# Optimization experiments

Measured on AMD Instinct MI355X. Metric: run time of the kernel, lower is better.

The kernel has to match this reference:

```python
import jax, jax.numpy as jnp
import numpy as np
from jax import lax

S, B, V, E, H = 512, 64, 50000, 400, 1150


def _lstm_layer(x, h0, c0, Wih, Whh, bih, bhh):
    # x: [S, B, Din]; PyTorch LSTM gate order: i, f, g, o
    WihT, WhhT = Wih.T, Whh.T

    def step(carry, xt):
        h, c = carry
        gates = xt @ WihT + bih + h @ WhhT + bhh  # [B, 4*Dh]
        i, f, g, o = jnp.split(gates, 4, axis=-1)
        c_new = jax.nn.sigmoid(f) * c + jax.nn.sigmoid(i) * jnp.tanh(g)
        h_new = jax.nn.sigmoid(o) * jnp.tanh(c_new)
        return (h_new, c_new), h_new

    (_, _), ys = lax.scan(step, (h0, c0), x)
    return ys  # [S, B, Dh]


def setup_inputs() -> dict:
    key = jax.random.key(0)

    def u(i, shape, s):
        return jax.random.uniform(jax.random.fold_in(key, i), shape, jnp.float32, -s, s)

    inp = {"tokens": jax.random.randint(jax.random.fold_in(key, 0), (S, B), 0, V)}
    inp["emb_w"] = u(1, (V, E), 0.1)  # encoder.weight.uniform_(-0.1, 0.1)
    dims = [(E, H), (H, H), (H, E)]  # (input_size, hidden_size) per layer
    k = 2
    for l, (din, dh) in enumerate(dims):
        s = 1.0 / float(np.sqrt(dh))
        inp[f"Wih{l}"] = u(k, (4 * dh, din), s); k += 1
        inp[f"Whh{l}"] = u(k, (4 * dh, dh), s); k += 1
        inp[f"bih{l}"] = u(k, (4 * dh,), s); k += 1
        inp[f"bhh{l}"] = u(k, (4 * dh,), s); k += 1
        inp[f"h{l}"] = jnp.zeros((B, dh), jnp.float32)
        inp[f"c{l}"] = jnp.zeros((B, dh), jnp.float32)
    return inp


def reference(tokens, emb_w, Wih0, Whh0, bih0, bhh0, Wih1, Whh1, bih1, bhh1,
              Wih2, Whh2, bih2, bhh2, h0, c0, h1, c1, h2, c2):
    # Eval-mode forward: embedding/locked/weight dropouts are identity.
    x = emb_w[tokens]  # [S, B, E]
    x = _lstm_layer(x, h0, c0, Wih0, Whh0, bih0, bhh0)  # [S, B, H]
    x = _lstm_layer(x, h1, c1, Wih1, Whh1, bih1, bhh1)  # [S, B, H]
    x = _lstm_layer(x, h2, c2, Wih2, Whh2, bih2, bhh2)  # [S, B, E]
    return x
```

## Files before the change

### kernel.cpp

```cpp
#include <hip/hip_runtime.h>
#include <hip/hip_bf16.h>
#include <cstdint>
#include <cstddef>


typedef _Float16 f16x8 __attribute__((ext_vector_type(8)));
typedef float f32x4 __attribute__((ext_vector_type(4)));
typedef unsigned int u32x4 __attribute__((ext_vector_type(4)));

#define LSTM_NBLK   241
#define LSTM_WSTEPS 515
#define LDS_W_HALFS (4 * 36 * 64 * 8)
#define LDS_TOTAL_BYTES (LDS_W_HALFS * 2 + 16384)
#define GO_BASE 248

struct KParams {
  const unsigned short* res[3];
  const unsigned short* strm[3];
  const float* bias[3];
  const unsigned short* xin0;
  unsigned short* ring[3];
  float* part;
  float* out;
  int* bar;
};

__device__ __forceinline__ float sigm_(float x) { return 1.0f / (1.0f + __expf(-x)); }
__device__ __forceinline__ float tanh_(float x) { return 2.0f * sigm_(2.0f * x) - 1.0f; }
__device__ __forceinline__ unsigned short f2h(float x) {
  _Float16 h = (_Float16)x;
  return __builtin_bit_cast(unsigned short, h);
}
__device__ __forceinline__ u32x4 load_sc(const unsigned short* p) {
  u32x4 r;
  asm volatile("global_load_dwordx4 %0, %1, off sc0 sc1"
               : "=v"(r) : "v"(p) : "memory");
  return r;
}
__device__ __forceinline__ f32x4 load_sc128f(const float* p) {
  f32x4 r;
  asm volatile("global_load_dwordx4 %0, %1, off sc0 sc1"
               : "=v"(r) : "v"(p) : "memory");
  return r;
}
__device__ __forceinline__ void store_sc128(unsigned short* p, u32x4 v) {
  asm volatile("global_store_dwordx4 %0, %1, off sc0 sc1" :: "v"(p), "v"(v) : "memory");
}
__device__ __forceinline__ void store_sc128f(float* p, f32x4 v) {
  asm volatile("global_store_dwordx4 %0, %1, off sc0 sc1" :: "v"(p), "v"(v) : "memory");
}
__device__ __forceinline__ void store_sc_i(int* p, int v) {
  asm volatile("global_store_dword %0, %1, off sc0 sc1" :: "v"(p), "v"(v) : "memory");
}
__device__ __forceinline__ int load_sc_i(const int* p) {
  int v;
  asm volatile("global_load_dword %0, %1, off sc0 sc1\n\ts_waitcnt vmcnt(0)"
               : "=v"(v) : "v"(p) : "memory");
  __builtin_amdgcn_sched_barrier(0);
  return v;
}
__device__ __forceinline__ void wait_vm0() {
  asm volatile("s_waitcnt vmcnt(0)" ::: "memory");
  __builtin_amdgcn_sched_barrier(0);
}

__device__ __forceinline__ void grid_barrier(int* bar, int bid, int tid, int tau1) {
  wait_vm0();
  __syncthreads();
  if (bid == 0) {
    if (tid >= 1 && tid < LSTM_NBLK) {
      int guard = 0;
      while (load_sc_i(&bar[tid * 32]) < tau1 && ++guard < (1 << 20))
        __builtin_amdgcn_s_sleep(1);
    }
    __syncthreads();
    if (tid < 8) store_sc_i(&bar[(GO_BASE + tid) * 32], tau1);
  } else {
    if (tid == 0) {
      store_sc_i(&bar[bid * 32], tau1);
      int guard = 0;
      while (load_sc_i(&bar[(GO_BASE + (bid & 7)) * 32]) < tau1 && ++guard < (1 << 20))
        __builtin_amdgcn_s_sleep(1);
    }
    __syncthreads();
  }
}

template<int L, int LAG>
__device__ __forceinline__ void run_layer(const KParams& p, int g, int bid,
                                          unsigned short* ldsW, float* gates) {
  constexpr int DH    = (L == 2) ? 400 : 1150;
  constexpr int NKB1  = (L == 0) ? 13 : 36;
  constexpr int NKB2  = (L == 2) ? 13 : 36;
  constexpr int XSTR  = (L == 0) ? 416 : 1152;
  constexpr int HSTR  = (L == 2) ? 416 : 1152;
  constexpr bool B1_RES = (L == 2);
  constexpr int NKB_ST = B1_RES ? NKB2 : NKB1;

  const unsigned short* __restrict__ strm = p.strm[L] + (size_t)g * (4 * NKB_ST * 512);
  const float* __restrict__ bias          = p.bias[L];
  const unsigned short* __restrict__ xin  = (L == 0) ? p.xin0 : p.ring[L - 1];
  unsigned short* __restrict__ own        = p.ring[L];

  const int tid  = threadIdx.x;
  const int lane = tid & 63;
  const int w    = tid >> 6;
  const int m0   = (w >> 2) << 4;
  const int kq   = w & 3;
  const int r    = lane & 15;
  const int q    = lane >> 4;

  {
    const uint4* src = (const uint4*)(p.res[L] + (size_t)g * LDS_W_HALFS);
    uint4* dst = (uint4*)ldsW;
    for (int i = tid; i < LDS_W_HALFS / 8; i += 1024) dst[i] = src[i];
#pragma unroll
    for (int s2 = 0; s2 < 4; ++s2) gates[s2 * 1024 + tid] = 0.0f;
  }

  const int b_ = tid >> 4;
  const int jp = tid & 15;
  const int jglob = g * 16 + jp;
  float bias4[4];
#pragma unroll
  for (int ss = 0; ss < 4; ++ss) bias4[ss] = bias[ss * 1152 + jglob];
  float c_val = 0.0f;
  __syncthreads();

  for (int tau = 0; tau < LSTM_WSTEPS; ++tau) {
    const int t = tau - LAG;
    if (t >= 0 && t < 512) {
      f32x4 acc[4] = {{0,0,0,0},{0,0,0,0},{0,0,0,0},{0,0,0,0}};

      const size_t slot1 = (L == 0) ? (size_t)t : (size_t)((t + 1) & 7);
      const unsigned short* a1base = xin + slot1 * (64 * XSTR) + (size_t)(m0 + r) * XSTR + q * 8;
      const unsigned short* a2base = own + (size_t)(t & 7) * (64 * HSTR) + (size_t)(m0 + r) * HSTR + q * 8;

      u32x4 a1r[9]; u32x4 a2r[9];
      if constexpr (L != 0) {
#pragma unroll
        for (int i = 0; i < 9; ++i) {
          int kb = kq + 4 * i;
          if (NKB1 == 36 || kb < NKB1) a1r[i] = load_sc(a1base + kb * 32);
        }
      }
#pragma unroll
      for (int i = 0; i < 9; ++i) {
        int kb = kq + 4 * i;
        if (i < ((NKB2 == 36) ? 9 : 4) && (NKB2 == 36 || kb < NKB2))
          a2r[i] = load_sc(a2base + kb * 32);
      }
      wait_vm0();

#pragma unroll
      for (int i = 0; i < ((NKB1 == 36) ? 9 : 4); ++i) {
        int kb = kq + 4 * i;
        if (NKB1 == 36 || kb < NKB1) {
          f16x8 a = (L == 0) ? *(const f16x8*)(a1base + kb * 32)
                             : __builtin_bit_cast(f16x8, a1r[i]);
#pragma unroll
          for (int s2 = 0; s2 < 4; ++s2) {
            f16x8 b = B1_RES
              ? *(const f16x8*)&ldsW[((s2 * 36 + kb) * 64 + lane) * 8]
              : *(const f16x8*)&strm[((size_t)(s2 * NKB_ST + kb) * 64 + lane) * 8];
            acc[s2] = __builtin_amdgcn_mfma_f32_16x16x32_f16(a, b, acc[s2], 0, 0, 0);
          }
        }
      }
#pragma unroll
      for (int i = 0; i < ((NKB2 == 36) ? 9 : 4); ++i) {
        int kb = kq + 4 * i;
        if (NKB2 == 36 || kb < NKB2) {
          f16x8 a = __builtin_bit_cast(f16x8, a2r[i]);
#pragma unroll
          for (int s2 = 0; s2 < 4; ++s2) {
            f16x8 b = B1_RES
              ? *(const f16x8*)&strm[((size_t)(s2 * NKB_ST + kb) * 64 + lane) * 8]
              : *(const f16x8*)&ldsW[((s2 * 36 + kb) * 64 + lane) * 8];
            acc[s2] = __builtin_amdgcn_mfma_f32_16x16x32_f16(a, b, acc[s2], 0, 0, 0);
          }
        }
      }

#pragma unroll
      for (int s2 = 0; s2 < 4; ++s2)
#pragma unroll
        for (int i = 0; i < 4; ++i)
          atomicAdd(&gates[s2 * 1024 + (m0 + q * 4 + i) * 16 + r], acc[s2][i]);
      __syncthreads();

      float pg[4];
#pragma unroll
      for (int s2 = 0; s2 < 4; ++s2) {
        pg[s2] = gates[s2 * 1024 + tid];
        gates[s2 * 1024 + tid] = 0.0f;
      }
      float ig = sigm_(pg[0] + bias4[0]);
      float fg = sigm_(pg[1] + bias4[1]);
      float gg = tanh_(pg[2] + bias4[2]);
      float og = sigm_(pg[3] + bias4[3]);
      c_val = fg * c_val + ig * gg;
      float h = og * tanh_(c_val);
      if (jglob >= DH) h = 0.0f;

      unsigned v0  = (unsigned)f2h(h);
      unsigned o1  = __shfl_down(v0, 1);
      unsigned p01 = v0 | (o1 << 16);
      unsigned o2  = __shfl_down(p01, 2);
      unsigned o4a = __shfl_down(p01, 4);
      unsigned o4b = __shfl_down(o2, 4);
      if ((lane & 7) == 0) {
        u32x4 pk; pk[0] = p01; pk[1] = o2; pk[2] = o4a; pk[3] = o4b;
        store_sc128(own + (size_t)(((t + 1) & 7) * 64 + b_) * HSTR + jglob, pk);
      }
      if (L == 2 && jglob < DH)
        p.out[((size_t)t * 64 + b_) * 400 + jglob] = h;
    }
    grid_barrier(p.bar, bid, tid, tau + 1);
  }
}

__device__ __forceinline__ void run_l1_ih(const KParams& p, int g, int bid,
                                          unsigned short* ldsW, float* gates) {
  const unsigned short* __restrict__ xin = p.ring[0];
  const int tid  = threadIdx.x;
  const int lane = tid & 63;
  const int w    = tid >> 6;
  const int m0   = (w >> 2) << 4;
  const int kq   = w & 3;
  const int r    = lane & 15;
  const int q    = lane >> 4;

  {
    const uint4* src = (const uint4*)(p.strm[1] + (size_t)g * LDS_W_HALFS);
    uint4* dst = (uint4*)ldsW;
    for (int i = tid; i < LDS_W_HALFS / 8; i += 1024) dst[i] = src[i];
#pragma unroll
    for (int s2 = 0; s2 < 4; ++s2) gates[s2 * 1024 + tid] = 0.0f;
  }
  __syncthreads();

  for (int tau = 0; tau < LSTM_WSTEPS; ++tau) {
    const int t = tau - 1;
    if (t >= 0 && t < 512) {
      f32x4 acc[4] = {{0,0,0,0},{0,0,0,0},{0,0,0,0},{0,0,0,0}};
      const unsigned short* a1base =
          xin + (size_t)((t + 1) & 7) * (64 * 1152) + (size_t)(m0 + r) * 1152 + q * 8;
      u32x4 a1r[9];
#pragma unroll
      for (int i = 0; i < 9; ++i) a1r[i] = load_sc(a1base + (kq + 4 * i) * 32);
      wait_vm0();
#pragma unroll
      for (int i = 0; i < 9; ++i) {
        int kb = kq + 4 * i;
        f16x8 a = __builtin_bit_cast(f16x8, a1r[i]);
#pragma unroll
        for (int s2 = 0; s2 < 4; ++s2) {
          f16x8 b = *(const f16x8*)&ldsW[((s2 * 36 + kb) * 64 + lane) * 8];
          acc[s2] = __builtin_amdgcn_mfma_f32_16x16x32_f16(a, b, acc[s2], 0, 0, 0);
        }
      }
#pragma unroll
      for (int s2 = 0; s2 < 4; ++s2)
#pragma unroll
        for (int i = 0; i < 4; ++i)
          atomicAdd(&gates[s2 * 1024 + (m0 + q * 4 + i) * 16 + r], acc[s2][i]);
      __syncthreads();
      f32x4 pk;
#pragma unroll
      for (int s2 = 0; s2 < 4; ++s2) {
        pk[s2] = gates[s2 * 1024 + tid];
        gates[s2 * 1024 + tid] = 0.0f;
      }
      store_sc128f(p.part + ((size_t)((t & 1) * 72 + g) * 1024 + tid) * 4, pk);
    }
    grid_barrier(p.bar, bid, tid, tau + 1);
  }
}

__device__ __forceinline__ void run_l1_hh(const KParams& p, int g, int bid,
                                          unsigned short* ldsW, float* gates) {
  unsigned short* __restrict__ own = p.ring[1];
  const int tid  = threadIdx.x;
  const int lane = tid & 63;
  const int w    = tid >> 6;
  const int m0   = (w >> 2) << 4;
  const int kq   = w & 3;
  const int r    = lane & 15;
  const int q    = lane >> 4;

  {
    const uint4* src = (const uint4*)(p.res[1] + (size_t)g * LDS_W_HALFS);
    uint4* dst = (uint4*)ldsW;
    for (int i = tid; i < LDS_W_HALFS / 8; i += 1024) dst[i] = src[i];
#pragma unroll
    for (int s2 = 0; s2 < 4; ++s2) gates[s2 * 1024 + tid] = 0.0f;
  }

  const int b_ = tid >> 4;
  const int jp = tid & 15;
  const int jglob = g * 16 + jp;
  float bias4[4];
#pragma unroll
  for (int ss = 0; ss < 4; ++ss) bias4[ss] = p.bias[1][ss * 1152 + jglob];
  float c_val = 0.0f;
  __syncthreads();

  for (int tau = 0; tau < LSTM_WSTEPS; ++tau) {
    const int t = tau - 2;
    if (t >= 0 && t < 512) {
      f32x4 acc[4] = {{0,0,0,0},{0,0,0,0},{0,0,0,0},{0,0,0,0}};
      const unsigned short* a2base =
          own + (size_t)(t & 7) * (64 * 1152) + (size_t)(m0 + r) * 1152 + q * 8;
      u32x4 a2r[9];
#pragma unroll
      for (int i = 0; i < 9; ++i) a2r[i] = load_sc(a2base + (kq + 4 * i) * 32);
      f32x4 pl = load_sc128f(p.part + ((size_t)((t & 1) * 72 + g) * 1024 + tid) * 4);
      wait_vm0();
#pragma unroll
      for (int i = 0; i < 9; ++i) {
        int kb = kq + 4 * i;
        f16x8 a = __builtin_bit_cast(f16x8, a2r[i]);
#pragma unroll
        for (int s2 = 0; s2 < 4; ++s2) {
          f16x8 b = *(const f16x8*)&ldsW[((s2 * 36 + kb) * 64 + lane) * 8];
          acc[s2] = __builtin_amdgcn_mfma_f32_16x16x32_f16(a, b, acc[s2], 0, 0, 0);
        }
      }
#pragma unroll
      for (int s2 = 0; s2 < 4; ++s2)
#pragma unroll
        for (int i = 0; i < 4; ++i)
          atomicAdd(&gates[s2 * 1024 + (m0 + q * 4 + i) * 16 + r], acc[s2][i]);
      __syncthreads();

      float pg[4];
#pragma unroll
      for (int s2 = 0; s2 < 4; ++s2) {
        pg[s2] = gates[s2 * 1024 + tid];
        gates[s2 * 1024 + tid] = 0.0f;
      }
      float ig = sigm_(pg[0] + pl[0] + bias4[0]);
      float fg = sigm_(pg[1] + pl[1] + bias4[1]);
      float gg = tanh_(pg[2] + pl[2] + bias4[2]);
      float og = sigm_(pg[3] + pl[3] + bias4[3]);
      c_val = fg * c_val + ig * gg;
      float h = og * tanh_(c_val);
      if (jglob >= 1150) h = 0.0f;

      unsigned v0  = (unsigned)f2h(h);
      unsigned o1  = __shfl_down(v0, 1);
      unsigned p01 = v0 | (o1 << 16);
      unsigned o2  = __shfl_down(p01, 2);
      unsigned o4a = __shfl_down(p01, 4);
      unsigned o4b = __shfl_down(o2, 4);
      if ((lane & 7) == 0) {
        u32x4 pk2; pk2[0] = p01; pk2[1] = o2; pk2[2] = o4a; pk2[3] = o4b;
        store_sc128(own + (size_t)(((t + 1) & 7) * 64 + b_) * 1152 + jglob, pk2);
      }
    }
    grid_barrier(p.bar, bid, tid, tau + 1);
  }
}

__global__ void __launch_bounds__(1024) lstm_persistent(KParams p) {
  extern __shared__ unsigned short smem[];
  unsigned short* ldsW = smem;
  float* gates = (float*)(smem + LDS_W_HALFS);
  const int bid = blockIdx.x;
  if (bid < 72)       run_layer<0, 0>(p, bid, bid, ldsW, gates);
  else if (bid < 144) run_l1_ih(p, bid - 72, bid, ldsW, gates);
  else if (bid < 216) run_l1_hh(p, bid - 144, bid, ldsW, gates);
  else                run_layer<2, 3>(p, bid - 216, bid, ldsW, gates);
}

__global__ void prep_weights(const float* __restrict__ src,
                             unsigned short* __restrict__ dst,
                             int Jext, int jg, int K, int NKB) {
  const int n = jg * 4 * NKB * 512;
  for (int idx = blockIdx.x * blockDim.x + threadIdx.x; idx < n;
       idx += gridDim.x * blockDim.x) {
    int e = idx & 7;
    int t2 = idx >> 3;
    int ln = t2 & 63; t2 >>= 6;
    int kb = t2 % NKB; t2 /= NKB;
    int s = t2 & 3;
    int g = t2 >> 2;
    int j = g * 16 + (ln & 15);
    int k = kb * 32 + (ln >> 4) * 8 + e;
    unsigned short v = 0;
    if (j < Jext && k < K) v = f2h(src[(size_t)(s * Jext + j) * K + k]);
    dst[idx] = v;
  }
}

__global__ void prep_bias(const float* __restrict__ bih,
                          const float* __restrict__ bhh,
                          float* __restrict__ dst, int Dh) {
  const int n = 4 * 1152;
  for (int idx = blockIdx.x * blockDim.x + threadIdx.x; idx < n;
       idx += gridDim.x * blockDim.x) {
    int s = idx / 1152, j = idx % 1152;
    float v = 0.0f;
    if (j < Dh) v = bih[s * Dh + j] + bhh[s * Dh + j];
    dst[idx] = v;
  }
}

__global__ void prep_gather(const int* __restrict__ tokens,
                            const float* __restrict__ emb,
                            unsigned short* __restrict__ xin0) {
  const int n = 512 * 64 * 52;
  for (int idx = blockIdx.x * blockDim.x + threadIdx.x; idx < n;
       idx += gridDim.x * blockDim.x) {
    int row = idx / 52;
    int cp  = idx - row * 52;
    unsigned short v[8] = {0, 0, 0, 0, 0, 0, 0, 0};
    if (cp < 50) {
      const float* src = emb + (size_t)tokens[row] * 400 + cp * 8;
      float4 a = *(const float4*)(src);
      float4 b = *(const float4*)(src + 4);
      v[0] = f2h(a.x); v[1] = f2h(a.y); v[2] = f2h(a.z); v[3] = f2h(a.w);
      v[4] = f2h(b.x); v[5] = f2h(b.y); v[6] = f2h(b.z); v[7] = f2h(b.w);
    }
    *(uint4*)(xin0 + (size_t)row * 416 + cp * 8) = *(const uint4*)v;
  }
}

extern "C" void kernel_launch(void* const* d_in, const int* in_sizes, int n_in,
                              void* d_out, int out_size, void* d_ws, size_t ws_size,
                              hipStream_t stream) {
  const int*   tokens = (const int*)d_in[0];
  const float* emb  = (const float*)d_in[1];
  const float* Wih0 = (const float*)d_in[2];
  const float* Whh0 = (const float*)d_in[3];
  const float* bih0 = (const float*)d_in[4];
  const float* bhh0 = (const float*)d_in[5];
  const float* Wih1 = (const float*)d_in[8];
  const float* Whh1 = (const float*)d_in[9];
  const float* bih1 = (const float*)d_in[10];
  const float* bhh1 = (const float*)d_in[11];
  const float* Wih2 = (const float*)d_in[14];
  const float* Whh2 = (const float*)d_in[15];
  const float* bih2 = (const float*)d_in[16];
  const float* bhh2 = (const float*)d_in[17];

  char* ws = (char*)d_ws;
  size_t off = 0;
  auto alloc = [&](size_t bytes) -> char* {
    char* ptr = ws + off;
    off += (bytes + 255) & ~(size_t)255;
    return ptr;
  };
  unsigned short* res0  = (unsigned short*)alloc(72ull * 4 * 36 * 512 * 2);
  unsigned short* res1  = (unsigned short*)alloc(72ull * 4 * 36 * 512 * 2);
  unsigned short* res2  = (unsigned short*)alloc(25ull * 4 * 36 * 512 * 2);
  unsigned short* strm0 = (unsigned short*)alloc(72ull * 4 * 13 * 512 * 2);
  unsigned short* strm1 = (unsigned short*)alloc(72ull * 4 * 36 * 512 * 2);
  unsigned short* strm2 = (unsigned short*)alloc(25ull * 4 * 13 * 512 * 2);
  float* bias0 = (float*)alloc(4ull * 1152 * 4);
  float* bias1 = (float*)alloc(4ull * 1152 * 4);
  float* bias2 = (float*)alloc(4ull * 1152 * 4);
  unsigned short* xin0  = (unsigned short*)alloc(512ull * 64 * 416 * 2);
  unsigned short* ring0 = (unsigned short*)alloc(8ull * 64 * 1152 * 2);
  unsigned short* ring1 = (unsigned short*)alloc(8ull * 64 * 1152 * 2);
  unsigned short* ring2 = (unsigned short*)alloc(8ull * 64 * 416 * 2);
  float* part = (float*)alloc(2ull * 72 * 1024 * 4 * 4);
  int* bar = (int*)alloc((GO_BASE + 8) * 32 * 4);
  if (off > ws_size) return;

  hipLaunchKernelGGL(prep_gather, dim3(2048), dim3(256), 0, stream, tokens, emb, xin0);
  hipLaunchKernelGGL(prep_weights, dim3(4096), dim3(256), 0, stream, Whh0, res0, 1150, 72, 1150, 36);
  hipLaunchKernelGGL(prep_weights, dim3(4096), dim3(256), 0, stream, Whh1, res1, 1150, 72, 1150, 36);
  hipLaunchKernelGGL(prep_weights, dim3(4096), dim3(256), 0, stream, Wih2, res2, 400, 25, 1150, 36);
  hipLaunchKernelGGL(prep_weights, dim3(4096), dim3(256), 0, stream, Wih0, strm0, 1150, 72, 400, 13);
  hipLaunchKernelGGL(prep_weights, dim3(4096), dim3(256), 0, stream, Wih1, strm1, 1150, 72, 1150, 36);
  hipLaunchKernelGGL(prep_weights, dim3(4096), dim3(256), 0, stream, Whh2, strm2, 400, 25, 400, 13);
  hipLaunchKernelGGL(prep_bias, dim3(8), dim3(256), 0, stream, bih0, bhh0, bias0, 1150);
  hipLaunchKernelGGL(prep_bias, dim3(8), dim3(256), 0, stream, bih1, bhh1, bias1, 1150);
  hipLaunchKernelGGL(prep_bias, dim3(8), dim3(256), 0, stream, bih2, bhh2, bias2, 400);
  (void)hipMemsetAsync(ring0, 0, 8ull * 64 * 1152 * 2, stream);
  (void)hipMemsetAsync(ring1, 0, 8ull * 64 * 1152 * 2, stream);
  (void)hipMemsetAsync(ring2, 0, 8ull * 64 * 416 * 2, stream);
  (void)hipMemsetAsync(bar, 0, (GO_BASE + 8) * 32 * 4, stream);

  KParams kp;
  kp.res[0] = res0;  kp.res[1] = res1;  kp.res[2] = res2;
  kp.strm[0] = strm0; kp.strm[1] = strm1; kp.strm[2] = strm2;
  kp.bias[0] = bias0; kp.bias[1] = bias1; kp.bias[2] = bias2;
  kp.xin0 = xin0;
  kp.ring[0] = ring0; kp.ring[1] = ring1; kp.ring[2] = ring2;
  kp.part = part;
  kp.out = (float*)d_out;
  kp.bar = bar;

  (void)hipFuncSetAttribute((const void*)lstm_persistent,
                            hipFuncAttributeMaxDynamicSharedMemorySize,
                            LDS_TOTAL_BYTES);
  hipLaunchKernelGGL(lstm_persistent, dim3(LSTM_NBLK), dim3(1024),
                     LDS_TOTAL_BYTES, stream, kp);
}
```

Measured before the change: 16.36 ms.

## Merge layer-1 input projection into layer-0 blocks to shrink persistent grid

Removes the 72 dedicated layer-1 input-projection blocks. Layer-0 blocks now also compute the previous step's h0 times Wih1 product, reusing the h0 fragments they already load, with the Wih1 weights streamed from global memory. This cuts the grid from 241 to 169 blocks, so fewer participants join each grid barrier. In exchange, each layer-0 block does more MFMA work, has extra syncthreads and streams more weights per step, which may lengthen the critical path of the layer-0 recurrence.

```diff
diff --git a/kernel.cpp b/kernel.cpp
--- a/kernel.cpp
+++ b/kernel.cpp
@@ -8,11 +8,11 @@
 typedef float f32x4 __attribute__((ext_vector_type(4)));
 typedef unsigned int u32x4 __attribute__((ext_vector_type(4)));
 
-#define LSTM_NBLK   241
+#define LSTM_NBLK   169
 #define LSTM_WSTEPS 515
 #define LDS_W_HALFS (4 * 36 * 64 * 8)
 #define LDS_TOTAL_BYTES (LDS_W_HALFS * 2 + 16384)
-#define GO_BASE 248
+#define GO_BASE 176
 
 struct KParams {
   const unsigned short* res[3];
@@ -86,21 +86,13 @@
   }
 }
 
-template<int L, int LAG>
-__device__ __forceinline__ void run_layer(const KParams& p, int g, int bid,
-                                          unsigned short* ldsW, float* gates) {
-  constexpr int DH    = (L == 2) ? 400 : 1150;
-  constexpr int NKB1  = (L == 0) ? 13 : 36;
-  constexpr int NKB2  = (L == 2) ? 13 : 36;
-  constexpr int XSTR  = (L == 0) ? 416 : 1152;
-  constexpr int HSTR  = (L == 2) ? 416 : 1152;
-  constexpr bool B1_RES = (L == 2);
-  constexpr int NKB_ST = B1_RES ? NKB2 : NKB1;
-
-  const unsigned short* __restrict__ strm = p.strm[L] + (size_t)g * (4 * NKB_ST * 512);
-  const float* __restrict__ bias          = p.bias[L];
-  const unsigned short* __restrict__ xin  = (L == 0) ? p.xin0 : p.ring[L - 1];
-  unsigned short* __restrict__ own        = p.ring[L];
+__device__ __forceinline__ void run_l0_merged(const KParams& p, int g, int bid,
+                                              unsigned short* ldsW, float* gates) {
+  const unsigned short* __restrict__ strmA = p.strm[0] + (size_t)g * (4 * 13 * 512);
+  const unsigned short* __restrict__ strmB = p.strm[1] + (size_t)g * (4 * 36 * 512);
+  const float* __restrict__ bias           = p.bias[0];
+  const unsigned short* __restrict__ xin   = p.xin0;
+  unsigned short* __restrict__ own         = p.ring[0];
 
   const int tid  = threadIdx.x;
   const int lane = tid & 63;
@@ -111,7 +103,7 @@
   const int q    = lane >> 4;
 
   {
-    const uint4* src = (const uint4*)(p.res[L] + (size_t)g * LDS_W_HALFS);
+    const uint4* src = (const uint4*)(p.res[0] + (size_t)g * LDS_W_HALFS);
     uint4* dst = (uint4*)ldsW;
     for (int i = tid; i < LDS_W_HALFS / 8; i += 1024) dst[i] = src[i];
 #pragma unroll
@@ -128,151 +120,110 @@
   __syncthreads();
 
   for (int tau = 0; tau < LSTM_WSTEPS; ++tau) {
-    const int t = tau - LAG;
-    if (t >= 0 && t < 512) {
-      f32x4 acc[4] = {{0,0,0,0},{0,0,0,0},{0,0,0,0},{0,0,0,0}};
-
-      const size_t slot1 = (L == 0) ? (size_t)t : (size_t)((t + 1) & 7);
-      const unsigned short* a1base = xin + slot1 * (64 * XSTR) + (size_t)(m0 + r) * XSTR + q * 8;
-      const unsigned short* a2base = own + (size_t)(t & 7) * (64 * HSTR) + (size_t)(m0 + r) * HSTR + q * 8;
-
-      u32x4 a1r[9]; u32x4 a2r[9];
-      if constexpr (L != 0) {
+    const bool doL0 = (tau < 512);
+    const bool doP  = (tau >= 1 && tau <= 512);
+    if (doL0 || doP) {
+      const unsigned short* a2base =
+          own + (size_t)(tau & 7) * (64 * 1152) + (size_t)(m0 + r) * 1152 + q * 8;
+      u32x4 a2r[9];
+#pragma unroll
+      for (int i = 0; i < 9; ++i) a2r[i] = load_sc(a2base + (kq + 4 * i) * 32);
+      wait_vm0();
+
+      f32x4 acc[4]  = {{0,0,0,0},{0,0,0,0},{0,0,0,0},{0,0,0,0}};
+      f32x4 pacc[4] = {{0,0,0,0},{0,0,0,0},{0,0,0,0},{0,0,0,0}};
+
+      if (doL0) {
+        const unsigned short* a1base =
+            xin + (size_t)tau * (64 * 416) + (size_t)(m0 + r) * 416 + q * 8;
+#pragma unroll
+        for (int i = 0; i < 4; ++i) {
+          int kb = kq + 4 * i;
+          if (kb < 13) {
+            f16x8 a = *(const f16x8*)(a1base + kb * 32);
+#pragma unroll
+            for (int s2 = 0; s2 < 4; ++s2) {
+              f16x8 b = *(const f16x8*)&strmA[((size_t)(s2 * 13 + kb) * 64 + lane) * 8];
+              acc[s2] = __builtin_amdgcn_mfma_f32_16x16x32_f16(a, b, acc[s2], 0, 0, 0);
+            }
+          }
+        }
 #pragma unroll
         for (int i = 0; i < 9; ++i) {
           int kb = kq + 4 * i;
-          if (NKB1 == 36 || kb < NKB1) a1r[i] = load_sc(a1base + kb * 32);
-        }
-      }
-#pragma unroll
-      for (int i = 0; i < 9; ++i) {
-        int kb = kq + 4 * i;
-        if (i < ((NKB2 == 36) ? 9 : 4) && (NKB2 == 36 || kb < NKB2))
-          a2r[i] = load_sc(a2base + kb * 32);
-      }
-      wait_vm0();
-
-#pragma unroll
-      for (int i = 0; i < ((NKB1 == 36) ? 9 : 4); ++i) {
-        int kb = kq + 4 * i;
-        if (NKB1 == 36 || kb < NKB1) {
-          f16x8 a = (L == 0) ? *(const f16x8*)(a1base + kb * 32)
-                             : __builtin_bit_cast(f16x8, a1r[i]);
+          f16x8 a = __builtin_bit_cast(f16x8, a2r[i]);
 #pragma unroll
           for (int s2 = 0; s2 < 4; ++s2) {
-            f16x8 b = B1_RES
-              ? *(const f16x8*)&ldsW[((s2 * 36 + kb) * 64 + lane) * 8]
-              : *(const f16x8*)&strm[((size_t)(s2 * NKB_ST + kb) * 64 + lane) * 8];
+            f16x8 b = *(const f16x8*)&ldsW[((s2 * 36 + kb) * 64 + lane) * 8];
             acc[s2] = __builtin_amdgcn_mfma_f32_16x16x32_f16(a, b, acc[s2], 0, 0, 0);
           }
         }
       }
-#pragma unroll
-      for (int i = 0; i < ((NKB2 == 36) ? 9 : 4); ++i) {
-        int kb = kq + 4 * i;
-        if (NKB2 == 36 || kb < NKB2) {
+      if (doP) {
+#pragma unroll
+        for (int i = 0; i < 9; ++i) {
+          int kb = kq + 4 * i;
           f16x8 a = __builtin_bit_cast(f16x8, a2r[i]);
 #pragma unroll
           for (int s2 = 0; s2 < 4; ++s2) {
-            f16x8 b = B1_RES
-              ? *(const f16x8*)&strm[((size_t)(s2 * NKB_ST + kb) * 64 + lane) * 8]
-              : *(const f16x8*)&ldsW[((s2 * 36 + kb) * 64 + lane) * 8];
-            acc[s2] = __builtin_amdgcn_mfma_f32_16x16x32_f16(a, b, acc[s2], 0, 0, 0);
+            f16x8 b = *(const f16x8*)&strmB[((size_t)(s2 * 36 + kb) * 64 + lane) * 8];
+            pacc[s2] = __builtin_amdgcn_mfma_f32_16x16x32_f16(a, b, pacc[s2], 0, 0, 0);
           }
         }
       }
 
-#pragma unroll
-      for (int s2 = 0; s2 < 4; ++s2)
-#pragma unroll
-        for (int i = 0; i < 4; ++i)
-          atomicAdd(&gates[s2 * 1024 + (m0 + q * 4 + i) * 16 + r], acc[s2][i]);
+      if (doL0) {
+#pragma unroll
+        for (int s2 = 0; s2 < 4; ++s2)
+#pragma unroll
+          for (int i = 0; i < 4; ++i)
+            atomicAdd(&gates[s2 * 1024 + (m0 + q * 4 + i) * 16 + r], acc[s2][i]);
+      }
       __syncthreads();
-
-      float pg[4];
-#pragma unroll
-      for (int s2 = 0; s2 < 4; ++s2) {
-        pg[s2] = gates[s2 * 1024 + tid];
-        gates[s2 * 1024 + tid] = 0.0f;
-      }
-      float ig = sigm_(pg[0] + bias4[0]);
-      float fg = sigm_(pg[1] + bias4[1]);
-      float gg = tanh_(pg[2] + bias4[2]);
-      float og = sigm_(pg[3] + bias4[3]);
-      c_val = fg * c_val + ig * gg;
-      float h = og * tanh_(c_val);
-      if (jglob >= DH) h = 0.0f;
-
-      unsigned v0  = (unsigned)f2h(h);
-      unsigned o1  = __shfl_down(v0, 1);
-      unsigned p01 = v0 | (o1 << 16);
-      unsigned o2  = __shfl_down(p01, 2);
-      unsigned o4a = __shfl_down(p01, 4);
-      unsigned o4b = __shfl_down(o2, 4);
-      if ((lane & 7) == 0) {
-        u32x4 pk; pk[0] = p01; pk[1] = o2; pk[2] = o4a; pk[3] = o4b;
-        store_sc128(own + (size_t)(((t + 1) & 7) * 64 + b_) * HSTR + jglob, pk);
-      }
-      if (L == 2 && jglob < DH)
-        p.out[((size_t)t * 64 + b_) * 400 + jglob] = h;
-    }
-    grid_barrier(p.bar, bid, tid, tau + 1);
-  }
-}
-
-__device__ __forceinline__ void run_l1_ih(const KParams& p, int g, int bid,
-                                          unsigned short* ldsW, float* gates) {
-  const unsigned short* __restrict__ xin = p.ring[0];
-  const int tid  = threadIdx.x;
-  const int lane = tid & 63;
-  const int w    = tid >> 6;
-  const int m0   = (w >> 2) << 4;
-  const int kq   = w & 3;
-  const int r    = lane & 15;
-  const int q    = lane >> 4;
-
-  {
-    const uint4* src = (const uint4*)(p.strm[1] + (size_t)g * LDS_W_HALFS);
-    uint4* dst = (uint4*)ldsW;
-    for (int i = tid; i < LDS_W_HALFS / 8; i += 1024) dst[i] = src[i];
-#pragma unroll
-    for (int s2 = 0; s2 < 4; ++s2) gates[s2 * 1024 + tid] = 0.0f;
-  }
-  __syncthreads();
-
-  for (int tau = 0; tau < LSTM_WSTEPS; ++tau) {
-    const int t = tau - 1;
-    if (t >= 0 && t < 512) {
-      f32x4 acc[4] = {{0,0,0,0},{0,0,0,0},{0,0,0,0},{0,0,0,0}};
-      const unsigned short* a1base =
-          xin + (size_t)((t + 1) & 7) * (64 * 1152) + (size_t)(m0 + r) * 1152 + q * 8;
-      u32x4 a1r[9];
-#pragma unroll
-      for (int i = 0; i < 9; ++i) a1r[i] = load_sc(a1base + (kq + 4 * i) * 32);
-      wait_vm0();
-#pragma unroll
-      for (int i = 0; i < 9; ++i) {
-        int kb = kq + 4 * i;
-        f16x8 a = __builtin_bit_cast(f16x8, a1r[i]);
+      if (doL0) {
+        float pg[4];
 #pragma unroll
         for (int s2 = 0; s2 < 4; ++s2) {
-          f16x8 b = *(const f16x8*)&ldsW[((s2 * 36 + kb) * 64 + lane) * 8];
-          acc[s2] = __builtin_amdgcn_mfma_f32_16x16x32_f16(a, b, acc[s2], 0, 0, 0);
-        }
-      }
-#pragma unroll
-      for (int s2 = 0; s2 < 4; ++s2)
-#pragma unroll
-        for (int i = 0; i < 4; ++i)
-          atomicAdd(&gates[s2 * 1024 + (m0 + q * 4 + i) * 16 + r], acc[s2][i]);
+          pg[s2] = gates[s2 * 1024 + tid];
+          gates[s2 * 1024 + tid] = 0.0f;
+        }
+        float ig = sigm_(pg[0] + bias4[0]);
+        float fg = sigm_(pg[1] + bias4[1]);
+        float gg = tanh_(pg[2] + bias4[2]);
+        float og = sigm_(pg[3] + bias4[3]);
+        c_val = fg * c_val + ig * gg;
+        float h = og * tanh_(c_val);
+        if (jglob >= 1150) h = 0.0f;
+
+        unsigned v0  = (unsigned)f2h(h);
+        unsigned o1  = __shfl_down(v0, 1);
+        unsigned p01 = v0 | (o1 << 16);
+        unsigned o2  = __shfl_down(p01, 2);
+        unsigned o4a = __shfl_down(p01, 4);
+        unsigned o4b = __shfl_down(o2, 4);
+        if ((lane & 7) == 0) {
+          u32x4 pk; pk[0] = p01; pk[1] = o2; pk[2] = o4a; pk[3] = o4b;
+          store_sc128(own + (size_t)(((tau + 1) & 7) * 64 + b_) * 1152 + jglob, pk);
+        }
+      }
       __syncthreads();
-      f32x4 pk;
-#pragma unroll
-      for (int s2 = 0; s2 < 4; ++s2) {
-        pk[s2] = gates[s2 * 1024 + tid];
-        gates[s2 * 1024 + tid] = 0.0f;
-      }
-      store_sc128f(p.part + ((size_t)((t & 1) * 72 + g) * 1024 + tid) * 4, pk);
+      if (doP) {
+#pragma unroll
+        for (int s2 = 0; s2 < 4; ++s2)
+#pragma unroll
+          for (int i = 0; i < 4; ++i)
+            atomicAdd(&gates[s2 * 1024 + (m0 + q * 4 + i) * 16 + r], pacc[s2][i]);
+      }
+      __syncthreads();
+      if (doP) {
+        f32x4 pk;
+#pragma unroll
+        for (int s2 = 0; s2 < 4; ++s2) {
+          pk[s2] = gates[s2 * 1024 + tid];
+          gates[s2 * 1024 + tid] = 0.0f;
+        }
+        store_sc128f(p.part + ((size_t)(((tau - 1) & 1) * 72 + g) * 1024 + tid) * 4, pk);
+      }
     }
     grid_barrier(p.bar, bid, tid, tau + 1);
   }
@@ -363,15 +314,125 @@
   }
 }
 
+__device__ __forceinline__ void run_l2(const KParams& p, int g, int bid,
+                                       unsigned short* ldsW, float* gates) {
+  const unsigned short* __restrict__ strm = p.strm[2] + (size_t)g * (4 * 13 * 512);
+  const unsigned short* __restrict__ xin  = p.ring[1];
+  unsigned short* __restrict__ own        = p.ring[2];
+
+  const int tid  = threadIdx.x;
+  const int lane = tid & 63;
+  const int w    = tid >> 6;
+  const int m0   = (w >> 2) << 4;
+  const int kq   = w & 3;
+  const int r    = lane & 15;
+  const int q    = lane >> 4;
+
+  {
+    const uint4* src = (const uint4*)(p.res[2] + (size_t)g * LDS_W_HALFS);
+    uint4* dst = (uint4*)ldsW;
+    for (int i = tid; i < LDS_W_HALFS / 8; i += 1024) dst[i] = src[i];
+#pragma unroll
+    for (int s2 = 0; s2 < 4; ++s2) gates[s2 * 1024 + tid] = 0.0f;
+  }
+
+  const int b_ = tid >> 4;
+  const int jp = tid & 15;
+  const int jglob = g * 16 + jp;
+  float bias4[4];
+#pragma unroll
+  for (int ss = 0; ss < 4; ++ss) bias4[ss] = p.bias[2][ss * 1152 + jglob];
+  float c_val = 0.0f;
+  __syncthreads();
+
+  for (int tau = 0; tau < LSTM_WSTEPS; ++tau) {
+    const int t = tau - 3;
+    if (t >= 0 && t < 512) {
+      f32x4 acc[4] = {{0,0,0,0},{0,0,0,0},{0,0,0,0},{0,0,0,0}};
+      const unsigned short* a1base =
+          xin + (size_t)((t + 1) & 7) * (64 * 1152) + (size_t)(m0 + r) * 1152 + q * 8;
+      const unsigned short* a2base =
+          own + (size_t)(t & 7) * (64 * 416) + (size_t)(m0 + r) * 416 + q * 8;
+
+      u32x4 a1r[9]; u32x4 a2r[4];
+#pragma unroll
+      for (int i = 0; i < 9; ++i) a1r[i] = load_sc(a1base + (kq + 4 * i) * 32);
+#pragma unroll
+      for (int i = 0; i < 4; ++i) {
+        int kb = kq + 4 * i;
+        if (kb < 13) a2r[i] = load_sc(a2base + kb * 32);
+      }
+      wait_vm0();
+
+#pragma unroll
+      for (int i = 0; i < 9; ++i) {
+        int kb = kq + 4 * i;
+        f16x8 a = __builtin_bit_cast(f16x8, a1r[i]);
+#pragma unroll
+        for (int s2 = 0; s2 < 4; ++s2) {
+          f16x8 b = *(const f16x8*)&ldsW[((s2 * 36 + kb) * 64 + lane) * 8];
+          acc[s2] = __builtin_amdgcn_mfma_f32_16x16x32_f16(a, b, acc[s2], 0, 0, 0);
+        }
+      }
+#pragma unroll
+      for (int i = 0; i < 4; ++i) {
+        int kb = kq + 4 * i;
+        if (kb < 13) {
+          f16x8 a = __builtin_bit_cast(f16x8, a2r[i]);
+#pragma unroll
+          for (int s2 = 0; s2 < 4; ++s2) {
+            f16x8 b = *(const f16x8*)&strm[((size_t)(s2 * 13 + kb) * 64 + lane) * 8];
+            acc[s2] = __builtin_amdgcn_mfma_f32_16x16x32_f16(a, b, acc[s2], 0, 0, 0);
+          }
+        }
+      }
+
+#pragma unroll
+      for (int s2 = 0; s2 < 4; ++s2)
+#pragma unroll
+        for (int i = 0; i < 4; ++i)
+          atomicAdd(&gates[s2 * 1024 + (m0 + q * 4 + i) * 16 + r], acc[s2][i]);
+      __syncthreads();
+
+      float pg[4];
+#pragma unroll
+      for (int s2 = 0; s2 < 4; ++s2) {
+        pg[s2] = gates[s2 * 1024 + tid];
+        gates[s2 * 1024 + tid] = 0.0f;
+      }
+      float ig = sigm_(pg[0] + bias4[0]);
+      float fg = sigm_(pg[1] + bias4[1]);
+      float gg = tanh_(pg[2] + bias4[2]);
+      float og = sigm_(pg[3] + bias4[3]);
+      c_val = fg * c_val + ig * gg;
+      float h = og * tanh_(c_val);
+      if (jglob >= 400) h = 0.0f;
+
+      unsigned v0  = (unsigned)f2h(h);
+      unsigned o1  = __shfl_down(v0, 1);
+      unsigned p01 = v0 | (o1 << 16);
+      unsigned o2  = __shfl_down(p01, 2);
+      unsigned o4a = __shfl_down(p01, 4);
+      unsigned o4b = __shfl_down(o2, 4);
+      if ((lane & 7) == 0) {
+        u32x4 pk; pk[0] = p01; pk[1] = o2; pk[2] = o4a; pk[3] = o4b;
+        store_sc128(own + (size_t)(((t + 1) & 7) * 64 + b_) * 416 + jglob, pk);
+      }
+      if (jglob < 400)
+        p.out[((size_t)t * 64 + b_) * 400 + jglob] = h;
+    }
+    grid_barrier(p.bar, bid, tid, tau + 1);
+  }
+}
+
 __global__ void __launch_bounds__(1024) lstm_persistent(KParams p) {
   extern __shared__ unsigned short smem[];
   unsigned short* ldsW = smem;
   float* gates = (float*)(smem + LDS_W_HALFS);
   const int bid = blockIdx.x;
-  if (bid < 72)       run_layer<0, 0>(p, bid, bid, ldsW, gates);
-  else if (bid < 144) run_l1_ih(p, bid - 72, bid, ldsW, gates);
-  else if (bid < 216) run_l1_hh(p, bid - 144, bid, ldsW, gates);
-  else                run_layer<2, 3>(p, bid - 216, bid, ldsW, gates);
+  if (bid < 72)       run_l0_merged(p, bid, bid, ldsW, gates);
+  else if (bid < 144) run_l1_hh(p, bid - 72, bid, ldsW, gates);
+  else                run_l2(p, bid - 144, bid, ldsW, gates);
 }
 
 __global__ void prep_weights(const float* __restrict__ src,
```

After: 36.87 ms. 2.25x slower.
